# Performance work log

Measured on AMD Instinct MI355X. Metric: run time of the kernel, lower is better.

## Reference

```python
import jax, jax.numpy as jnp
import numpy as np

N_NODES = 50000
DEG = 16
N_EDGES = N_NODES * DEG
IN_FEATS = 256
NUM_HEADS = 4
OUT_FEATS = 64
NEG_SLOPE = 0.2


def setup_inputs() -> dict:
    key = jax.random.key(0)
    k1, k2, k3, k4, k5, k6 = jax.random.split(key, 6)
    row_ptr = jnp.arange(N_NODES + 1, dtype=jnp.int64 if jax.config.jax_enable_x64 else jnp.int32) * DEG
    col_ind = jax.random.randint(k1, (N_EDGES,), 0, N_NODES)
    # CSC mirrors (used only by the fused op's backward pass; math-inert here)
    col_ptr = jnp.arange(N_NODES + 1, dtype=row_ptr.dtype) * DEG
    row_ind = jax.random.randint(k2, (N_EDGES,), 0, N_NODES)
    feat = jax.random.normal(k3, (N_NODES, IN_FEATS), dtype=jnp.float32)
    # Glorot-style init for params
    g = float(np.sqrt(2.0))  # gain for relu
    std_W = g * np.sqrt(2.0 / (IN_FEATS + OUT_FEATS * NUM_HEADS))
    W = jax.random.normal(k4, (IN_FEATS, OUT_FEATS * NUM_HEADS), dtype=jnp.float32) * std_W
    std_a = g * np.sqrt(2.0 / (1 + NUM_HEADS * OUT_FEATS))
    attn_l = jax.random.normal(k5, (1, NUM_HEADS, OUT_FEATS), dtype=jnp.float32) * std_a
    attn_r = jax.random.normal(k6, (1, NUM_HEADS, OUT_FEATS), dtype=jnp.float32) * std_a
    return {"row_ptr": row_ptr, "col_ind": col_ind, "col_ptr": col_ptr,
            "row_ind": row_ind, "feat": feat, "W": W, "attn_l": attn_l, "attn_r": attn_r}


def reference(row_ptr, col_ind, col_ptr, row_ind, feat, W, attn_l, attn_r):
    N = feat.shape[0]
    E = col_ind.shape[0]
    # Dense projection: [N, H, F]
    h = jnp.matmul(feat, W).reshape(N, NUM_HEADS, OUT_FEATS)
    attn_row = jnp.sum(attn_l * h, axis=-1)  # [N, H] (dst scores)
    attn_col = jnp.sum(attn_r * h, axis=-1)  # [N, H] (src scores)
    # Recover destination node id per edge from CSR row_ptr
    dst = jnp.searchsorted(row_ptr, jnp.arange(E), side="right") - 1  # [E]
    src = col_ind  # [E]
    # Edge score: LeakyReLU(attn_row[dst] + attn_col[src])
    e = attn_row[dst] + attn_col[src]  # [E, H]
    e = jnp.where(e > 0, e, NEG_SLOPE * e)
    # Segment softmax over each destination's neighborhood
    e_max = jax.ops.segment_max(e, dst, num_segments=N)  # [N, H]
    ex = jnp.exp(e - e_max[dst])  # [E, H]
    denom = jax.ops.segment_sum(ex, dst, num_segments=N)  # [N, H]
    alpha = ex / denom[dst]  # [E, H]
    # Weighted scatter-add aggregation of source features
    out = jax.ops.segment_sum(h[src] * alpha[:, :, None], dst, num_segments=N)  # [N, H, F]
    return out
```

## Files before the change

### kernel.cpp

```cpp
#include <hip/hip_runtime.h>
#include <hip/hip_bf16.h>

#define DEG        16
#define IN_FEATS   256
#define NUM_HEADS  4
#define OUT_FEATS  64
#define HF         256
#define NEG_SLOPE  0.2f

#define CPITCH 264

typedef __attribute__((ext_vector_type(8))) short  short8;
typedef __attribute__((ext_vector_type(4))) float  floatx4;
typedef unsigned short ushortT;

__device__ __forceinline__ unsigned short f2bf(float f) {
    union { float f; unsigned u; } v; v.f = f;
    unsigned r = v.u + 0x7fffu + ((v.u >> 16) & 1u);
    return (unsigned short)(r >> 16);
}
__device__ __forceinline__ float bf_lo(unsigned u) {
    union { unsigned x; float f; } v; v.x = u << 16; return v.f;
}
__device__ __forceinline__ float bf_hi(unsigned u) {
    union { unsigned x; float f; } v; v.x = u & 0xffff0000u; return v.f;
}
__device__ __forceinline__ unsigned cvt2(float lo, float hi) {
    return (unsigned)f2bf(lo) | ((unsigned)f2bf(hi) << 16);
}

__global__ __launch_bounds__(256) void conv_wt(
    const float* __restrict__ W, ushortT* __restrict__ Wt)
{
    int n = blockIdx.x;
    int k = threadIdx.x;
    Wt[n * 256 + k] = f2bf(W[k * 256 + n]);
}

__global__ __launch_bounds__(256, 3) void gat_gemm_fused(
    const float* __restrict__ feat,
    const ushortT* __restrict__ Bt,
    const float* __restrict__ attn_l,
    const float* __restrict__ attn_r,
    ushortT* __restrict__ Hb,
    float* __restrict__ arow,
    float* __restrict__ acol,
    int M)
{
    __shared__ __align__(16) ushortT SMEM[64 * CPITCH];
    ushortT* As = SMEM;
    ushortT* Cs = SMEM;

    const int tid  = threadIdx.x;
    const int wave = tid >> 6;
    const int lane = tid & 63;
    const int l15  = lane & 15;
    const int quad = lane >> 4;
    const int rowBase = blockIdx.x * 64;

    short8 bbuf[2][4];
    #pragma unroll
    for (int ni = 0; ni < 4; ++ni)
        bbuf[0][ni] = *(const short8*)&Bt[(wave * 64 + ni * 16 + l15) * 256 + quad * 8];

    #pragma unroll
    for (int pass = 0; pass < 2; ++pass) {
        float4 v[8];
        #pragma unroll
        for (int i = 0; i < 8; ++i) {
            int id  = pass * 2048 + i * 256 + tid;
            int row = id >> 6;
            int c4  = id & 63;
            int gr  = rowBase + row; if (gr > M - 1) gr = M - 1;
            v[i] = *(const float4*)&feat[(size_t)gr * 256 + c4 * 4];
        }
        #pragma unroll
        for (int i = 0; i < 8; ++i) {
            int id   = pass * 2048 + i * 256 + tid;
            int row  = id >> 6;
            int c4   = id & 63;
            int cg   = c4 >> 1;
            int half = c4 & 1;
            uint2 w = make_uint2(cvt2(v[i].x, v[i].y), cvt2(v[i].z, v[i].w));
            *(uint2*)&As[row * 256 + ((cg ^ (row & 7)) << 3) + half * 4] = w;
        }
    }

    __syncthreads();

    floatx4 acc[4][4] = {};

    #pragma unroll
    for (int ks = 0; ks < 8; ++ks) {
        if (ks < 7) {
            #pragma unroll
            for (int ni = 0; ni < 4; ++ni)
                bbuf[(ks + 1) & 1][ni] = *(const short8*)
                    &Bt[(wave * 64 + ni * 16 + l15) * 256 + (ks + 1) * 32 + quad * 8];
        }
        short8 af[4];
        #pragma unroll
        for (int mi = 0; mi < 4; ++mi) {
            int row = mi * 16 + l15;
            int q   = ks * 4 + quad;
            int cst = q ^ (row & 7);
            af[mi] = *(const short8*)&As[row * 256 + cst * 8];
        }
        #pragma unroll
        for (int mi = 0; mi < 4; ++mi)
            #pragma unroll
            for (int ni = 0; ni < 4; ++ni)
                acc[mi][ni] = __builtin_amdgcn_mfma_f32_16x16x32_bf16(
                    af[mi], bbuf[ks & 1][ni], acc[mi][ni], 0, 0, 0);
    }

    float al[4], ar[4];
    #pragma unroll
    for (int ni = 0; ni < 4; ++ni) {
        al[ni] = attn_l[wave * 64 + ni * 16 + l15];
        ar[ni] = attn_r[wave * 64 + ni * 16 + l15];
    }
    #pragma unroll
    for (int mi = 0; mi < 4; ++mi) {
        #pragma unroll
        for (int reg = 0; reg < 4; ++reg) {
            float pl = 0.f, pr = 0.f;
            #pragma unroll
            for (int ni = 0; ni < 4; ++ni) {
                pl = fmaf(acc[mi][ni][reg], al[ni], pl);
                pr = fmaf(acc[mi][ni][reg], ar[ni], pr);
            }
            #pragma unroll
            for (int off = 8; off >= 1; off >>= 1) {
                pl += __shfl_xor(pl, off, 64);
                pr += __shfl_xor(pr, off, 64);
            }
            if (l15 == 0) {
                int gr = rowBase + mi * 16 + quad * 4 + reg;
                if (gr < M) {
                    arow[gr * NUM_HEADS + wave] = pl;
                    acol[gr * NUM_HEADS + wave] = pr;
                }
            }
        }
    }

    __syncthreads();

    #pragma unroll
    for (int mi = 0; mi < 4; ++mi)
        #pragma unroll
        for (int ni = 0; ni < 4; ++ni)
            #pragma unroll
            for (int reg = 0; reg < 4; ++reg)
                Cs[(mi * 16 + quad * 4 + reg) * CPITCH + wave * 64 + ni * 16 + l15] =
                    f2bf(acc[mi][ni][reg]);
    __syncthreads();

    #pragma unroll
    for (int i = 0; i < 8; ++i) {
        int f  = tid + 256 * i;
        int r  = f >> 5;
        int c8 = (f & 31) << 3;
        int gr = rowBase + r;
        if (gr < M) {
            uint4 v = *(const uint4*)&Cs[r * CPITCH + c8];
            *(uint4*)&Hb[(size_t)gr * HF + c8] = v;
        }
    }
}

__global__ __launch_bounds__(256) void gat_aggregate5(
    const ushortT* __restrict__ Hb,
    const float* __restrict__ arow,
    const float* __restrict__ acol,
    const int* __restrict__ col_ind,
    float* __restrict__ out,
    int N)
{
    const int tid  = threadIdx.x;
    const int wave = tid >> 6;
    const int lane = tid & 63;
    const int n    = blockIdx.x * 4 + wave;
    if (n >= N) return;

    const int j16  = lane & 15;
    const int hd16 = lane >> 4;

    int   src_e = col_ind[n * DEG + j16];
    float e = arow[n * NUM_HEADS + hd16] + acol[src_e * NUM_HEADS + hd16];
    e = (e > 0.f) ? e : NEG_SLOPE * e;

    float m = e;
    #pragma unroll
    for (int off = 8; off >= 1; off >>= 1)
        m = fmaxf(m, __shfl_xor(m, off, 16));
    float ex = __expf(e - m);
    float s = ex;
    #pragma unroll
    for (int off = 8; off >= 1; off >>= 1)
        s += __shfl_xor(s, off, 16);
    float alpha = ex / s;

    const int l32     = lane & 31;
    const int half    = lane >> 5;
    const int headSel = (l32 >> 3) << 4;

    int   sj[8];
    float av[8];
    #pragma unroll
    for (int j = 0; j < 8; ++j) {
        int ep = (j << 1) + half;
        sj[j] = __shfl(src_e, ep, 64);
        av[j] = __shfl(alpha, headSel + ep, 64);
    }

    uint4 v[8];
    #pragma unroll
    for (int j = 0; j < 8; ++j)
        v[j] = *(const uint4*)&Hb[(size_t)sj[j] * HF + l32 * 8];

    __builtin_amdgcn_sched_barrier(0);

    float acc[8] = {};
    #pragma unroll
    for (int j = 0; j < 8; ++j) {
        acc[0] = fmaf(av[j], bf_lo(v[j].x), acc[0]);
        acc[1] = fmaf(av[j], bf_hi(v[j].x), acc[1]);
        acc[2] = fmaf(av[j], bf_lo(v[j].y), acc[2]);
        acc[3] = fmaf(av[j], bf_hi(v[j].y), acc[3]);
        acc[4] = fmaf(av[j], bf_lo(v[j].z), acc[4]);
        acc[5] = fmaf(av[j], bf_hi(v[j].z), acc[5]);
        acc[6] = fmaf(av[j], bf_lo(v[j].w), acc[6]);
        acc[7] = fmaf(av[j], bf_hi(v[j].w), acc[7]);
    }

    #pragma unroll
    for (int i = 0; i < 8; ++i)
        acc[i] += __shfl_xor(acc[i], 32, 64);

    float4 o;
    if (half == 0) o = make_float4(acc[0], acc[1], acc[2], acc[3]);
    else           o = make_float4(acc[4], acc[5], acc[6], acc[7]);
    *(float4*)&out[(size_t)n * HF + l32 * 8 + half * 4] = o;
}

extern "C" void kernel_launch(void* const* d_in, const int* in_sizes, int n_in,
                              void* d_out, int out_size, void* d_ws, size_t ws_size,
                              hipStream_t stream) {
    const int*   col_ind = (const int*)  d_in[1];
    const float* feat    = (const float*)d_in[4];
    const float* W       = (const float*)d_in[5];
    const float* attn_l  = (const float*)d_in[6];
    const float* attn_r  = (const float*)d_in[7];
    float* out = (float*)d_out;

    const int N = in_sizes[0] - 1;

    ushortT* Hb   = (ushortT*)d_ws;
    float*   arow = (float*)(Hb + (size_t)N * HF);
    float*   acol = arow + (size_t)N * NUM_HEADS;
    ushortT* Wt   = (ushortT*)(acol + (size_t)N * NUM_HEADS);

    conv_wt<<<256, 256, 0, stream>>>(W, Wt);

    dim3 ggrid((N + 63) / 64);
    gat_gemm_fused<<<ggrid, 256, 0, stream>>>(feat, Wt, attn_l, attn_r,
                                              Hb, arow, acol, N);

    gat_aggregate5<<<(N + 3) / 4, 256, 0, stream>>>(Hb, arow, acol, col_ind, out, N);
}
```

Before: 191.1 us.

## Make aggregation kernel persistent with prefetch of next node's indices and scores

The aggregation kernel becomes a grid-stride persistent kernel with a fixed number of blocks (7 per CU across 256 CUs). Each wave software-pipelines by loading col_ind two nodes ahead and the arow/acol scores one node ahead, so the dependent index-then-score load chain is hidden behind the current node's gather. Output stores are marked nontemporal to avoid polluting cache with write-only data. In exchange it holds more registers per wave and has fewer waves in flight for latency hiding than launching one wave per node.

```diff
diff --git a/kernel.cpp b/kernel.cpp
--- a/kernel.cpp
+++ b/kernel.cpp
@@ -170,79 +170,100 @@
     }
 }
 
-__global__ __launch_bounds__(256) void gat_aggregate5(
+__global__ __launch_bounds__(256, 7) void gat_aggregate6(
     const ushortT* __restrict__ Hb,
     const float* __restrict__ arow,
     const float* __restrict__ acol,
     const int* __restrict__ col_ind,
     float* __restrict__ out,
-    int N)
+    int N, int NW)
 {
     const int tid  = threadIdx.x;
     const int wave = tid >> 6;
     const int lane = tid & 63;
-    const int n    = blockIdx.x * 4 + wave;
-    if (n >= N) return;
 
     const int j16  = lane & 15;
     const int hd16 = lane >> 4;
-
-    int   src_e = col_ind[n * DEG + j16];
-    float e = arow[n * NUM_HEADS + hd16] + acol[src_e * NUM_HEADS + hd16];
-    e = (e > 0.f) ? e : NEG_SLOPE * e;
-
-    float m = e;
-    #pragma unroll
-    for (int off = 8; off >= 1; off >>= 1)
-        m = fmaxf(m, __shfl_xor(m, off, 16));
-    float ex = __expf(e - m);
-    float s = ex;
-    #pragma unroll
-    for (int off = 8; off >= 1; off >>= 1)
-        s += __shfl_xor(s, off, 16);
-    float alpha = ex / s;
-
     const int l32     = lane & 31;
     const int half    = lane >> 5;
     const int headSel = (l32 >> 3) << 4;
 
-    int   sj[8];
-    float av[8];
-    #pragma unroll
-    for (int j = 0; j < 8; ++j) {
-        int ep = (j << 1) + half;
-        sj[j] = __shfl(src_e, ep, 64);
-        av[j] = __shfl(alpha, headSel + ep, 64);
-    }
-
-    uint4 v[8];
-    #pragma unroll
-    for (int j = 0; j < 8; ++j)
-        v[j] = *(const uint4*)&Hb[(size_t)sj[j] * HF + l32 * 8];
-
-    __builtin_amdgcn_sched_barrier(0);
-
-    float acc[8] = {};
-    #pragma unroll
-    for (int j = 0; j < 8; ++j) {
-        acc[0] = fmaf(av[j], bf_lo(v[j].x), acc[0]);
-        acc[1] = fmaf(av[j], bf_hi(v[j].x), acc[1]);
-        acc[2] = fmaf(av[j], bf_lo(v[j].y), acc[2]);
-        acc[3] = fmaf(av[j], bf_hi(v[j].y), acc[3]);
-        acc[4] = fmaf(av[j], bf_lo(v[j].z), acc[4]);
-        acc[5] = fmaf(av[j], bf_hi(v[j].z), acc[5]);
-        acc[6] = fmaf(av[j], bf_lo(v[j].w), acc[6]);
-        acc[7] = fmaf(av[j], bf_hi(v[j].w), acc[7]);
-    }
-
-    #pragma unroll
-    for (int i = 0; i < 8; ++i)
-        acc[i] += __shfl_xor(acc[i], 32, 64);
-
-    float4 o;
-    if (half == 0) o = make_float4(acc[0], acc[1], acc[2], acc[3]);
-    else           o = make_float4(acc[4], acc[5], acc[6], acc[7]);
-    *(float4*)&out[(size_t)n * HF + l32 * 8 + half * 4] = o;
+    int n = blockIdx.x * 4 + wave;
+    if (n >= N) return;
+
+    int srcCur = col_ind[n * DEG + j16];
+    int n1g    = n + NW;
+    int srcNext = col_ind[((n1g < N) ? n1g : n) * DEG + j16];
+    float arCur = arow[n * NUM_HEADS + hd16];
+    float acCur = acol[srcCur * NUM_HEADS + hd16];
+
+    while (n < N) {
+        const int n1 = n + NW;
+        const int n2 = n1 + NW;
+
+        int srcN2 = srcNext;
+        if (n2 < N) srcN2 = col_ind[n2 * DEG + j16];
+
+        float arNext = arCur, acNext = acCur;
+        if (n1 < N) {
+            arNext = arow[n1 * NUM_HEADS + hd16];
+            acNext = acol[srcNext * NUM_HEADS + hd16];
+        }
+
+        float e = arCur + acCur;
+        e = (e > 0.f) ? e : NEG_SLOPE * e;
+        float m = e;
+        #pragma unroll
+        for (int off = 8; off >= 1; off >>= 1)
+            m = fmaxf(m, __shfl_xor(m, off, 16));
+        float ex = __expf(e - m);
+        float s = ex;
+        #pragma unroll
+        for (int off = 8; off >= 1; off >>= 1)
+            s += __shfl_xor(s, off, 16);
+        float alpha = ex / s;
+
+        int   sj[8];
+        float av[8];
+        #pragma unroll
+        for (int j = 0; j < 8; ++j) {
+            int ep = (j << 1) + half;
+            sj[j] = __shfl(srcCur, ep, 64);
+            av[j] = __shfl(alpha, headSel + ep, 64);
+        }
+        uint4 v[8];
+        #pragma unroll
+        for (int j = 0; j < 8; ++j)
+            v[j] = *(const uint4*)&Hb[(size_t)sj[j] * HF + l32 * 8];
+
+        __builtin_amdgcn_sched_barrier(0);
+
+        float acc[8] = {};
+        #pragma unroll
+        for (int j = 0; j < 8; ++j) {
+            acc[0] = fmaf(av[j], bf_lo(v[j].x), acc[0]);
+            acc[1] = fmaf(av[j], bf_hi(v[j].x), acc[1]);
+            acc[2] = fmaf(av[j], bf_lo(v[j].y), acc[2]);
+            acc[3] = fmaf(av[j], bf_hi(v[j].y), acc[3]);
+            acc[4] = fmaf(av[j], bf_lo(v[j].z), acc[4]);
+            acc[5] = fmaf(av[j], bf_hi(v[j].z), acc[5]);
+            acc[6] = fmaf(av[j], bf_lo(v[j].w), acc[6]);
+            acc[7] = fmaf(av[j], bf_hi(v[j].w), acc[7]);
+        }
+        #pragma unroll
+        for (int i = 0; i < 8; ++i)
+            acc[i] += __shfl_xor(acc[i], 32, 64);
+
+        floatx4 o;
+        if (half == 0) { o.x = acc[0]; o.y = acc[1]; o.z = acc[2]; o.w = acc[3]; }
+        else           { o.x = acc[4]; o.y = acc[5]; o.z = acc[6]; o.w = acc[7]; }
+        __builtin_nontemporal_store(
+            o, (floatx4*)&out[(size_t)n * HF + l32 * 8 + half * 4]);
+
+        srcCur = srcNext; srcNext = srcN2;
+        arCur  = arNext;  acCur   = acNext;
+        n = n1;
+    }
 }
 
 extern "C" void kernel_launch(void* const* d_in, const int* in_sizes, int n_in,
@@ -268,5 +289,9 @@
     gat_gemm_fused<<<ggrid, 256, 0, stream>>>(feat, Wt, attn_l, attn_r,
                                               Hb, arow, acol, N);
 
-    gat_aggregate5<<<(N + 3) / 4, 256, 0, stream>>>(Hb, arow, acol, col_ind, out, N);
-}
+    int nblocks = 7 * 256;
+    int maxb = (N + 3) / 4;
+    if (nblocks > maxb) nblocks = maxb;
+    int NW = nblocks * 4;
+    gat_aggregate6<<<nblocks, 256, 0, stream>>>(Hb, arow, acol, col_ind, out, N, NW);
+}
```

Measured after the change: 347.4 us. 1.82x slower.
